# Optimization experiments

Hardware: AMD Instinct MI355X
Metric: run time of the kernel (lower is better)

Reference implementation:

```python
import jax, jax.numpy as jnp
import numpy as np

B, S, D = 4, 2048, 1024          # batch, seq, hidden_units
E, K, I = 16, 2, 1024            # n_routed_experts, top_k, moe_inter_dim
SH = 2                            # n_shared_experts -> shared inter = SH*I
ROUTE_SCALE = 1.0


def setup_inputs() -> dict:
    key = jax.random.key(0)
    ks = jax.random.split(key, 12)
    std = 0.02
    return {
        "x": jax.random.normal(ks[0], (B, S, D), jnp.float32),
        "gate_w": jax.random.normal(ks[1], (E, D), jnp.float32) * std,
        # expert weights, torch Linear layout [out, in], stacked over experts
        "w1": jax.random.normal(ks[2], (E, I, D), jnp.float32) * std,
        "w2": jax.random.normal(ks[3], (E, D, I), jnp.float32) * std,
        "w3": jax.random.normal(ks[4], (E, I, D), jnp.float32) * std,
        # shared expert MLP (bias=True, nn.Linear default)
        "sw1": jax.random.normal(ks[5], (SH * I, D), jnp.float32) * std,
        "sb1": jnp.zeros((SH * I,), jnp.float32),
        "sw2": jax.random.normal(ks[6], (D, SH * I), jnp.float32) * std,
        "sb2": jnp.zeros((D,), jnp.float32),
        "sw3": jax.random.normal(ks[7], (SH * I, D), jnp.float32) * std,
        "sb3": jnp.zeros((SH * I,), jnp.float32),
    }


def reference(x, gate_w, w1, w2, w3, sw1, sb1, sw2, sb2, sw3, sb3):
    orig_shape = x.shape
    xt = x.reshape(-1, D)                       # [T, D]
    T = xt.shape[0]

    # ---- Gate: sigmoid scores, top-k, normalized weights ----
    scores = jax.nn.sigmoid(xt @ gate_w.T)      # [T, E]
    topk_vals, topk_idx = jax.lax.top_k(scores, K)
    weights = topk_vals / topk_vals.sum(-1, keepdims=True) * ROUTE_SCALE  # [T, K]

    # dense per-token-per-expert combine weight (zero for unselected experts)
    onehot = jax.nn.one_hot(topk_idx, E, dtype=xt.dtype)  # [T, K, E]
    w_full = jnp.einsum('tk,tke->te', weights, onehot)    # [T, E]

    # ---- Routed experts: SwiGLU per expert, weighted combine ----
    y = jnp.zeros_like(xt)
    for e in range(E):  # fixed small structural loop over experts
        h = jax.nn.silu(xt @ w1[e].T) * (xt @ w3[e].T)    # [T, I]
        y = y + w_full[:, e:e + 1] * (h @ w2[e].T)

    # ---- Load-balancing auxiliary loss ----
    counts = jax.lax.stop_gradient(onehot.sum((0, 1)))    # tokens per expert (non-diff, as in torch)
    expert_probs = w_full.sum(0)                          # sum of routing weights per expert
    f_i = E * counts / (K * T)
    P_i = expert_probs / T
    L_ExpBal = (f_i * P_i).sum()

    # ---- Shared expert (dense SwiGLU MLP with bias) ----
    z = (jax.nn.silu(xt @ sw1.T + sb1) * (xt @ sw3.T + sb3)) @ sw2.T + sb2

    return (y + z).reshape(orig_shape), L_ExpBal
```

## Files before the change

kernel.cpp:

```cpp
#include <hip/hip_runtime.h>
#include <cstdint>
#include <cstddef>

typedef unsigned short ushort_t;
typedef __attribute__((ext_vector_type(8))) short bf16x8;
typedef __attribute__((ext_vector_type(8))) unsigned short u16x8;
typedef __attribute__((ext_vector_type(4))) float f32x4;

#define T_TOKENS 8192
#define DIM      1024
#define NEXP     16

static __device__ __forceinline__ unsigned short f2bf(float f) {
  union { float f; unsigned u; } v; v.f = f;
  unsigned r = v.u + 0x7FFFu + ((v.u >> 16) & 1u);
  return (unsigned short)(r >> 16);
}

static __device__ __forceinline__ void gload16(const void* g, void* l) {
  __builtin_amdgcn_global_load_lds(
      (const __attribute__((address_space(1))) unsigned int*)g,
      (__attribute__((address_space(3))) unsigned int*)l, 16, 0, 0);
}

static __device__ __forceinline__ void xcd_map(int bx, int by, int gy,
                                               int& rb, int& cb) {
  int lin = bx + (by << 6);
  int xcd = lin & 7;
  int c = lin >> 3;
  int gyd = gy >> 3;
  cb = xcd * gyd + (c >> 6);
  rb = c & 63;
}

__global__ __launch_bounds__(256) void k_cvt8(const float* __restrict__ in,
                                              ushort_t* __restrict__ outp) {
  size_t i = ((size_t)blockIdx.x * 256 + threadIdx.x) * 8;
  float4 a = *(const float4*)(in + i);
  float4 b = *(const float4*)(in + i + 4);
  u16x8 o;
  o[0]=f2bf(a.x); o[1]=f2bf(a.y); o[2]=f2bf(a.z); o[3]=f2bf(a.w);
  o[4]=f2bf(b.x); o[5]=f2bf(b.y); o[6]=f2bf(b.z); o[7]=f2bf(b.w);
  *(u16x8*)(outp + i) = o;
}

__global__ __launch_bounds__(256) void k_score(const float* __restrict__ x,
                                               const float* __restrict__ gw,
                                               int* __restrict__ sel0,
                                               int* __restrict__ sel1,
                                               float* __restrict__ w0o,
                                               float* __restrict__ w1o) {
  int lane = threadIdx.x & 63;
  int wv = threadIdx.x >> 6;
  int t = blockIdx.x * 4 + wv;
  float xv[16];
  const float* xr = x + (size_t)t * DIM + lane * 16;
#pragma unroll
  for (int j = 0; j < 16; j += 4) {
    float4 v = *(const float4*)(xr + j);
    xv[j] = v.x; xv[j+1] = v.y; xv[j+2] = v.z; xv[j+3] = v.w;
  }
  float sc[NEXP];
#pragma unroll
  for (int e = 0; e < NEXP; e++) {
    const float* gr = gw + (size_t)e * DIM + lane * 16;
    float a = 0.f;
#pragma unroll
    for (int j = 0; j < 16; j += 4) {
      float4 g = *(const float4*)(gr + j);
      a += xv[j]*g.x + xv[j+1]*g.y + xv[j+2]*g.z + xv[j+3]*g.w;
    }
#pragma unroll
    for (int o = 32; o > 0; o >>= 1) a += __shfl_xor(a, o, 64);
    sc[e] = 1.f / (1.f + expf(-a));
  }
  if (lane == 0) {
    float best = -1e30f, sec = -1e30f;
    int bi = 0, si = 0;
#pragma unroll
    for (int e = 0; e < NEXP; e++) {
      float s = sc[e];
      if (s > best) { sec = best; si = bi; best = s; bi = e; }
      else if (s > sec) { sec = s; si = e; }
    }
    float inv = 1.f / (best + sec);
    sel0[t] = bi; sel1[t] = si;
    w0o[t] = best * inv; w1o[t] = sec * inv;
  }
}

__global__ __launch_bounds__(256) void k_compact(const int* __restrict__ sel0,
                                                 const int* __restrict__ sel1,
                                                 const float* __restrict__ w0v,
                                                 const float* __restrict__ w1v,
                                                 int* __restrict__ toklist,
                                                 float* __restrict__ wlist,
                                                 int* __restrict__ cnt,
                                                 float* __restrict__ probs) {
  const int e = blockIdx.x;
  const int tid = threadIdx.x;
  const int lane = tid & 63, wv = tid >> 6;
  __shared__ int wbase[4];
  __shared__ int woff[4];
  __shared__ int base;
  __shared__ float pacc[4];
  if (tid == 0) base = 0;
  float myprob = 0.f;
  int* tl = toklist + e * T_TOKENS;
  float* wl = wlist + e * T_TOKENS;
  __syncthreads();
  for (int t0 = 0; t0 < T_TOKENS; t0 += 256) {
    int t = t0 + tid;
    bool m0 = (sel0[t] == e), m1 = (sel1[t] == e);
    bool m = m0 || m1;
    float wgt = m0 ? w0v[t] : (m1 ? w1v[t] : 0.f);
    unsigned long long bal = __ballot(m);
    int prefix = __popcll(bal & ((1ull << lane) - 1ull));
    if (lane == 0) wbase[wv] = __popcll(bal);
    __syncthreads();
    if (tid == 0) {
      int a = base;
#pragma unroll
      for (int i = 0; i < 4; i++) { woff[i] = a; a += wbase[i]; }
      base = a;
    }
    __syncthreads();
    if (m) {
      int pos = woff[wv] + prefix;
      tl[pos] = t;
      wl[pos] = wgt;
    }
    myprob += wgt;
  }
#pragma unroll
  for (int o = 32; o > 0; o >>= 1) myprob += __shfl_xor(myprob, o, 64);
  if (lane == 0) pacc[wv] = myprob;
  __syncthreads();
  if (tid == 0) {
    cnt[e] = base;
    probs[e] = pacc[0] + pacc[1] + pacc[2] + pacc[3];
  }
}

__global__ void k_offsets(const int* __restrict__ cnt, const float* __restrict__ probs,
                          int* __restrict__ seg, float* __restrict__ loss_out) {
  if (threadIdx.x == 0 && blockIdx.x == 0) {
    int acc = 0;
    float L = 0.f;
    for (int e = 0; e < NEXP; e++) {
      seg[e] = acc; acc += cnt[e];
      float f = 16.f * (float)cnt[e] / (2.f * 8192.f);
      L += f * (probs[e] / 8192.f);
    }
    seg[NEXP] = acc;
    *loss_out = L;
  }
}


__global__ __launch_bounds__(256, 3) void k_gemm1(
    const ushort_t* __restrict__ X,
    const ushort_t* __restrict__ W1b, const ushort_t* __restrict__ W3b,
    const float* __restrict__ b1, const float* __restrict__ b3,
    ushort_t* __restrict__ P, int ldP,
    const int* __restrict__ toklist, const int* __restrict__ cnt,
    const int* __restrict__ seg) {
  __shared__ __align__(16) ushort_t As[2 * 4096];
  __shared__ __align__(16) ushort_t B1s[2 * 2048];
  __shared__ __align__(16) ushort_t B3s[2 * 2048];

  const int tid = threadIdx.x;
  const int lane = tid & 63, wave = tid >> 6;
  const int wm = wave >> 1, wn = wave & 1;
  int rb, cb;
  xcd_map(blockIdx.x, blockIdx.y, gridDim.y, rb, cb);
  const int e = blockIdx.z;

  int Ne, pbase;
  const int* tl = nullptr;
  const ushort_t* W1 = W1b;
  const ushort_t* W3 = W3b;
  if (cnt) {
    Ne = cnt[e];
    if (rb * 128 >= Ne) return;
    pbase = seg[e];
    tl = toklist + e * T_TOKENS;
    W1 += (size_t)e * 1024 * 1024;
    W3 += (size_t)e * 1024 * 1024;
  } else { Ne = T_TOKENS; pbase = 0; }

  const int c0 = wave * 2, c1 = c0 + 1;
  const int lrow = lane >> 2;
  const int scol = (((lane & 3) ^ (lrow & 3))) * 8;

  const int ar0 = rb * 128 + c0 * 16 + lrow;
  const int ar1 = rb * 128 + c1 * 16 + lrow;
  const int sr0 = tl ? tl[min(ar0, Ne - 1)] : ar0;
  const int sr1 = tl ? tl[min(ar1, Ne - 1)] : ar1;
  const ushort_t* apA0 = X + (size_t)sr0 * DIM + scol;
  const ushort_t* apA1 = X + (size_t)sr1 * DIM + scol;

  const int brw = cb * 64 + wave * 16 + lrow;
  const ushort_t* bp1 = W1 + (size_t)brw * DIM + scol;
  const ushort_t* bp3 = W3 + (size_t)brw * DIM + scol;

  const int o0 = c0 * 512, o1 = c1 * 512;
  const int ow = wave * 512;

  f32x4 acc1[4][2], acc3[4][2];
#pragma unroll
  for (int m = 0; m < 4; m++)
#pragma unroll
    for (int n = 0; n < 2; n++) {
      acc1[m][n] = (f32x4){0.f, 0.f, 0.f, 0.f};
      acc3[m][n] = (f32x4){0.f, 0.f, 0.f, 0.f};
    }

  const int koff = (((lane >> 4) ^ (lane & 3))) * 8;

#define STAGE1(AB, BB, K0) { \
    gload16(apA0 + (K0), As  + (AB) + o0); \
    gload16(apA1 + (K0), As  + (AB) + o1); \
    gload16(bp1  + (K0), B1s + (BB) + ow); \
    gload16(bp3  + (K0), B3s + (BB) + ow); }

#define PHASE1(AC, BC, T, STG) { \
    if (STG) STAGE1(4096 - (AC), 2048 - (BC), ((T) + 1) * 32); \
    bf16x8 af[4], b1f[2], b3f[2]; \
    _Pragma("unroll") \
    for (int m = 0; m < 4; m++) { \
      int row = wm * 64 + m * 16 + (lane & 15); \
      af[m] = *(const bf16x8*)(As + (AC) + row * 32 + koff); } \
    _Pragma("unroll") \
    for (int n = 0; n < 2; n++) { \
      int rw = wn * 32 + n * 16 + (lane & 15); \
      b1f[n] = *(const bf16x8*)(B1s + (BC) + rw * 32 + koff); \
      b3f[n] = *(const bf16x8*)(B3s + (BC) + rw * 32 + koff); } \
    _Pragma("unroll") \
    for (int m = 0; m < 4; m++) \
      _Pragma("unroll") \
      for (int n = 0; n < 2; n++) { \
        acc1[m][n] = __builtin_amdgcn_mfma_f32_16x16x32_bf16(af[m], b1f[n], acc1[m][n], 0, 0, 0); \
        acc3[m][n] = __builtin_amdgcn_mfma_f32_16x16x32_bf16(af[m], b3f[n], acc3[m][n], 0, 0, 0); } \
    __syncthreads(); }

  STAGE1(0, 0, 0);
  __syncthreads();
  for (int kk = 0; kk < 30; kk += 2) {
    PHASE1(0, 0, kk, 1);
    PHASE1(4096, 2048, kk + 1, 1);
  }
  PHASE1(0, 0, 30, 1);
  PHASE1(4096, 2048, 31, 0);
#undef PHASE1
#undef STAGE1

#pragma unroll
  for (int n = 0; n < 2; n++) {
    int col = cb * 64 + wn * 32 + n * 16 + (lane & 15);
    float bb1 = b1 ? b1[col] : 0.f;
    float bb3 = b3 ? b3[col] : 0.f;
#pragma unroll
    for (int m = 0; m < 4; m++) {
#pragma unroll
      for (int r = 0; r < 4; r++) {
        int row = rb * 128 + wm * 64 + m * 16 + (lane >> 4) * 4 + r;
        if (row < Ne) {
          float h1 = acc1[m][n][r] + bb1;
          float h3 = acc3[m][n][r] + bb3;
          float pv = (h1 / (1.f + expf(-h1))) * h3;
          P[(size_t)(pbase + row) * ldP + col] = f2bf(pv);
        }
      }
    }
  }
}

__global__ __launch_bounds__(256, 3) void k_gemm2(
    const ushort_t* __restrict__ Pbuf, const ushort_t* __restrict__ W2b,
    const float* __restrict__ b2,
    float* __restrict__ outp,
    const int* __restrict__ toklist, const float* __restrict__ wlist,
    const int* __restrict__ cnt, const int* __restrict__ seg, int Kd) {
  __shared__ __align__(16) ushort_t As[2 * 4096];
  __shared__ __align__(16) ushort_t Bs[2 * 4096];

  const int tid = threadIdx.x;
  const int lane = tid & 63, wave = tid >> 6;
  const int wm = wave >> 1, wn = wave & 1;
  int rb, cb;
  xcd_map(blockIdx.x, blockIdx.y, gridDim.y, rb, cb);
  const int e = blockIdx.z;

  int Ne;
  const ushort_t* A;
  const ushort_t* W2 = W2b;
  const int* tl = nullptr; const float* wl = nullptr;
  if (cnt) {
    Ne = cnt[e];
    if (rb * 128 >= Ne) return;
    A = Pbuf + (size_t)seg[e] * Kd;
    W2 += (size_t)e * 1024 * Kd;
    tl = toklist + e * T_TOKENS;
    wl = wlist + e * T_TOKENS;
  } else { Ne = T_TOKENS; A = Pbuf; }

  const int c0 = wave * 2, c1 = c0 + 1;
  const int lrow = lane >> 2;
  const int scol = (((lane & 3) ^ (lrow & 3))) * 8;

  const int sr0 = min(rb * 128 + c0 * 16 + lrow, Ne - 1);
  const int sr1 = min(rb * 128 + c1 * 16 + lrow, Ne - 1);
  const ushort_t* apA0 = A + (size_t)sr0 * Kd + scol;
  const ushort_t* apA1 = A + (size_t)sr1 * Kd + scol;

  const int br0 = cb * 128 + c0 * 16 + lrow;
  const int br1 = cb * 128 + c1 * 16 + lrow;
  const ushort_t* bp0 = W2 + (size_t)br0 * Kd + scol;
  const ushort_t* bp1 = W2 + (size_t)br1 * Kd + scol;

  const int o0 = c0 * 512, o1 = c1 * 512;

  f32x4 acc[4][4];
#pragma unroll
  for (int m = 0; m < 4; m++)
#pragma unroll
    for (int n = 0; n < 4; n++) acc[m][n] = (f32x4){0.f, 0.f, 0.f, 0.f};

  const int koff = (((lane >> 4) ^ (lane & 3))) * 8;
  const int ksteps = Kd >> 5;

#define STAGE2(BUF, K0) { \
    gload16(apA0 + (K0), As + (BUF) + o0); \
    gload16(apA1 + (K0), As + (BUF) + o1); \
    gload16(bp0  + (K0), Bs + (BUF) + o0); \
    gload16(bp1  + (K0), Bs + (BUF) + o1); }

#define PHASE2(CUR, T, STG) { \
    if (STG) STAGE2(4096 - (CUR), ((T) + 1) * 32); \
    bf16x8 af[4], bf[4]; \
    _Pragma("unroll") \
    for (int m = 0; m < 4; m++) { \
      int row = wm * 64 + m * 16 + (lane & 15); \
      af[m] = *(const bf16x8*)(As + (CUR) + row * 32 + koff); } \
    _Pragma("unroll") \
    for (int n = 0; n < 4; n++) { \
      int rw = wn * 64 + n * 16 + (lane & 15); \
      bf[n] = *(const bf16x8*)(Bs + (CUR) + rw * 32 + koff); } \
    _Pragma("unroll") \
    for (int m = 0; m < 4; m++) \
      _Pragma("unroll") \
      for (int n = 0; n < 4; n++) \
        acc[m][n] = __builtin_amdgcn_mfma_f32_16x16x32_bf16(af[m], bf[n], acc[m][n], 0, 0, 0); \
    __syncthreads(); }

  STAGE2(0, 0);
  __syncthreads();
  for (int kk = 0; kk < ksteps - 2; kk += 2) {
    PHASE2(0, kk, 1);
    PHASE2(4096, kk + 1, 1);
  }
  PHASE2(0, ksteps - 2, 1);
  PHASE2(4096, ksteps - 1, 0);
#undef PHASE2
#undef STAGE2

#pragma unroll
  for (int n = 0; n < 4; n++) {
    int col = cb * 128 + wn * 64 + n * 16 + (lane & 15);
    float bias = b2 ? b2[col] : 0.f;
#pragma unroll
    for (int m = 0; m < 4; m++) {
#pragma unroll
      for (int r = 0; r < 4; r++) {
        int rl = rb * 128 + wm * 64 + m * 16 + (lane >> 4) * 4 + r;
        if (cnt) {
          if (rl < Ne) {
            int tok = tl[rl];
            float wgt = wl[rl];
            atomicAdd(outp + (size_t)tok * DIM + col, acc[m][n][r] * wgt);
          }
        } else {
          outp[(size_t)rl * DIM + col] = acc[m][n][r] + bias;
        }
      }
    }
  }
}

extern "C" void kernel_launch(void* const* d_in, const int* in_sizes, int n_in,
                              void* d_out, int out_size, void* d_ws, size_t ws_size,
                              hipStream_t stream) {
  const float* x   = (const float*)d_in[0];
  const float* gw  = (const float*)d_in[1];
  const float* w1  = (const float*)d_in[2];
  const float* w2  = (const float*)d_in[3];
  const float* w3  = (const float*)d_in[4];
  const float* sw1 = (const float*)d_in[5];
  const float* sb1 = (const float*)d_in[6];
  const float* sw2 = (const float*)d_in[7];
  const float* sb2 = (const float*)d_in[8];
  const float* sw3 = (const float*)d_in[9];
  const float* sb3 = (const float*)d_in[10];
  float* out  = (float*)d_out;
  float* loss = out + (size_t)T_TOKENS * DIM;

  const size_t NW = (size_t)NEXP * 1024 * 1024;
  const size_t NS = (size_t)2048 * 1024;

  char* w = (char*)d_ws;
  ushort_t* w1b  = (ushort_t*)w; w += NW * 2;
  ushort_t* w2b  = (ushort_t*)w; w += NW * 2;
  ushort_t* w3b  = (ushort_t*)w; w += NW * 2;
  ushort_t* sw1b = (ushort_t*)w; w += NS * 2;
  ushort_t* sw2b = (ushort_t*)w; w += NS * 2;
  ushort_t* sw3b = (ushort_t*)w; w += NS * 2;
  ushort_t* p_buf = (ushort_t*)w; w += (size_t)33554432 + 262144;
  ushort_t* x_bf  = (ushort_t*)w; w += (size_t)T_TOKENS * DIM * 2;
  int*   toklist  = (int*)w;      w += (size_t)NEXP * T_TOKENS * 4;
  float* wlist    = (float*)w;    w += (size_t)NEXP * T_TOKENS * 4;
  int*   sel0     = (int*)w;      w += (size_t)T_TOKENS * 4;
  int*   sel1     = (int*)w;      w += (size_t)T_TOKENS * 4;
  float* w0v      = (float*)w;    w += (size_t)T_TOKENS * 4;
  float* w1v      = (float*)w;    w += (size_t)T_TOKENS * 4;
  int*   cnt      = (int*)w;      w += 64;
  float* probs    = (float*)w;    w += 64;
  int*   seg      = (int*)w;      w += 128;

  k_cvt8<<<(T_TOKENS * DIM) / 2048, 256, 0, stream>>>(x, x_bf);
  k_cvt8<<<NW / 2048, 256, 0, stream>>>(w1, w1b);
  k_cvt8<<<NW / 2048, 256, 0, stream>>>(w2, w2b);
  k_cvt8<<<NW / 2048, 256, 0, stream>>>(w3, w3b);
  k_cvt8<<<NS / 2048, 256, 0, stream>>>(sw1, sw1b);
  k_cvt8<<<NS / 2048, 256, 0, stream>>>(sw2, sw2b);
  k_cvt8<<<NS / 2048, 256, 0, stream>>>(sw3, sw3b);

  k_score<<<T_TOKENS / 4, 256, 0, stream>>>(x, gw, sel0, sel1, w0v, w1v);
  k_compact<<<NEXP, 256, 0, stream>>>(sel0, sel1, w0v, w1v,
                                      toklist, wlist, cnt, probs);
  k_offsets<<<1, 64, 0, stream>>>(cnt, probs, seg, loss);

  k_gemm1<<<dim3(64, 32, 1), 256, 0, stream>>>(x_bf, sw1b, sw3b, sb1, sb3,
                                               p_buf, 2048, nullptr, nullptr, nullptr);
  k_gemm2<<<dim3(64, 8, 1), 256, 0, stream>>>(p_buf, sw2b, sb2, out,
                                              nullptr, nullptr, nullptr, nullptr, 2048);

  k_gemm1<<<dim3(64, 16, NEXP), 256, 0, stream>>>(x_bf, w1b, w3b, nullptr, nullptr,
                                                  p_buf, 1024, toklist, cnt, seg);
  k_gemm2<<<dim3(64, 8, NEXP), 256, 0, stream>>>(p_buf, w2b, nullptr, out,
                                                 toklist, wlist, cnt, seg, 1024);
}
```

Measured before the change: 596.2 us.

## Merge conversion launches and fuse shared-expert GEMMs into routed-expert grids

Replaces seven separate fp32-to-bf16 conversion launches with one kernel that picks the source tensor by block index. Folds the shared-expert GEMMs into the routed-expert launches as an extra z-slice, giving each a separate intermediate buffer when workspace allows. The output is zeroed up front and every slice accumulates with atomics. This removes launch overhead and tail idle time between the shared and routed phases, at the cost of an extra memset and atomic stores for the shared expert's output.

Measured after the change: 608.9 us. 2.1% more time.

```diff
diff --git a/kernel.cpp b/kernel.cpp
--- a/kernel.cpp
+++ b/kernel.cpp
@@ -33,15 +33,31 @@
   rb = c & 63;
 }
 
-__global__ __launch_bounds__(256) void k_cvt8(const float* __restrict__ in,
-                                              ushort_t* __restrict__ outp) {
-  size_t i = ((size_t)blockIdx.x * 256 + threadIdx.x) * 8;
-  float4 a = *(const float4*)(in + i);
-  float4 b = *(const float4*)(in + i + 4);
+__global__ __launch_bounds__(256) void k_cvt_all(
+    const float* __restrict__ x,  const float* __restrict__ w1,
+    const float* __restrict__ w2, const float* __restrict__ w3,
+    const float* __restrict__ sw1, const float* __restrict__ sw2,
+    const float* __restrict__ sw3,
+    ushort_t* __restrict__ xb,  ushort_t* __restrict__ w1b,
+    ushort_t* __restrict__ w2b, ushort_t* __restrict__ w3b,
+    ushort_t* __restrict__ sw1b, ushort_t* __restrict__ sw2b,
+    ushort_t* __restrict__ sw3b) {
+  int b = blockIdx.x;
+  const float* src; ushort_t* dst; int rel;
+  if (b < 4096)       { src = x;   dst = xb;   rel = b; }
+  else if (b < 12288) { src = w1;  dst = w1b;  rel = b - 4096; }
+  else if (b < 20480) { src = w2;  dst = w2b;  rel = b - 12288; }
+  else if (b < 28672) { src = w3;  dst = w3b;  rel = b - 20480; }
+  else if (b < 29696) { src = sw1; dst = sw1b; rel = b - 28672; }
+  else if (b < 30720) { src = sw2; dst = sw2b; rel = b - 29696; }
+  else                { src = sw3; dst = sw3b; rel = b - 30720; }
+  size_t i = ((size_t)rel * 256 + threadIdx.x) * 8;
+  float4 a = *(const float4*)(src + i);
+  float4 c = *(const float4*)(src + i + 4);
   u16x8 o;
   o[0]=f2bf(a.x); o[1]=f2bf(a.y); o[2]=f2bf(a.z); o[3]=f2bf(a.w);
-  o[4]=f2bf(b.x); o[5]=f2bf(b.y); o[6]=f2bf(b.z); o[7]=f2bf(b.w);
-  *(u16x8*)(outp + i) = o;
+  o[4]=f2bf(c.x); o[5]=f2bf(c.y); o[6]=f2bf(c.z); o[7]=f2bf(c.w);
+  *(u16x8*)(dst + i) = o;
 }
 
 __global__ __launch_bounds__(256) void k_score(const float* __restrict__ x,
@@ -157,14 +173,14 @@
   }
 }
 
-
 __global__ __launch_bounds__(256, 3) void k_gemm1(
     const ushort_t* __restrict__ X,
-    const ushort_t* __restrict__ W1b, const ushort_t* __restrict__ W3b,
-    const float* __restrict__ b1, const float* __restrict__ b3,
-    ushort_t* __restrict__ P, int ldP,
+    const ushort_t* __restrict__ w1b, const ushort_t* __restrict__ w3b,
+    const ushort_t* __restrict__ sw1b, const ushort_t* __restrict__ sw3b,
+    const float* __restrict__ sb1, const float* __restrict__ sb3,
+    ushort_t* __restrict__ Pr, ushort_t* __restrict__ Ps,
     const int* __restrict__ toklist, const int* __restrict__ cnt,
-    const int* __restrict__ seg) {
+    const int* __restrict__ seg, int zbase) {
   __shared__ __align__(16) ushort_t As[2 * 4096];
   __shared__ __align__(16) ushort_t B1s[2 * 2048];
   __shared__ __align__(16) ushort_t B3s[2 * 2048];
@@ -172,22 +188,29 @@
   const int tid = threadIdx.x;
   const int lane = tid & 63, wave = tid >> 6;
   const int wm = wave >> 1, wn = wave & 1;
-  int rb, cb;
-  xcd_map(blockIdx.x, blockIdx.y, gridDim.y, rb, cb);
-  const int e = blockIdx.z;
-
-  int Ne, pbase;
+  const int e = blockIdx.z + zbase;
+
+  int rb, cb, Ne, pbase, ldP;
   const int* tl = nullptr;
-  const ushort_t* W1 = W1b;
-  const ushort_t* W3 = W3b;
-  if (cnt) {
+  const ushort_t *W1, *W3;
+  const float *b1 = nullptr, *b3 = nullptr;
+  ushort_t* P;
+  if (e < NEXP) {
+    if (blockIdx.y >= 16) return;
+    xcd_map(blockIdx.x, blockIdx.y, 16, rb, cb);
     Ne = cnt[e];
     if (rb * 128 >= Ne) return;
     pbase = seg[e];
     tl = toklist + e * T_TOKENS;
-    W1 += (size_t)e * 1024 * 1024;
-    W3 += (size_t)e * 1024 * 1024;
-  } else { Ne = T_TOKENS; pbase = 0; }
+    W1 = w1b + (size_t)e * 1024 * 1024;
+    W3 = w3b + (size_t)e * 1024 * 1024;
+    P = Pr; ldP = 1024;
+  } else {
+    xcd_map(blockIdx.x, blockIdx.y, 32, rb, cb);
+    Ne = T_TOKENS; pbase = 0;
+    W1 = sw1b; W3 = sw3b; b1 = sb1; b3 = sb3;
+    P = Ps; ldP = 2048;
+  }
 
   const int c0 = wave * 2, c1 = c0 + 1;
   const int lrow = lane >> 2;
@@ -277,33 +300,38 @@
 }
 
 __global__ __launch_bounds__(256, 3) void k_gemm2(
-    const ushort_t* __restrict__ Pbuf, const ushort_t* __restrict__ W2b,
-    const float* __restrict__ b2,
+    const ushort_t* __restrict__ Pr, const ushort_t* __restrict__ Ps,
+    const ushort_t* __restrict__ w2b, const ushort_t* __restrict__ sw2b,
+    const float* __restrict__ sb2,
     float* __restrict__ outp,
     const int* __restrict__ toklist, const float* __restrict__ wlist,
-    const int* __restrict__ cnt, const int* __restrict__ seg, int Kd) {
+    const int* __restrict__ cnt, const int* __restrict__ seg, int zbase) {
   __shared__ __align__(16) ushort_t As[2 * 4096];
   __shared__ __align__(16) ushort_t Bs[2 * 4096];
 
   const int tid = threadIdx.x;
   const int lane = tid & 63, wave = tid >> 6;
   const int wm = wave >> 1, wn = wave & 1;
+  const int e = blockIdx.z + zbase;
   int rb, cb;
-  xcd_map(blockIdx.x, blockIdx.y, gridDim.y, rb, cb);
-  const int e = blockIdx.z;
-
-  int Ne;
-  const ushort_t* A;
-  const ushort_t* W2 = W2b;
+  xcd_map(blockIdx.x, blockIdx.y, 8, rb, cb);
+
+  int Ne, Kd;
+  const ushort_t *A, *W2;
   const int* tl = nullptr; const float* wl = nullptr;
-  if (cnt) {
+  const float* b2 = nullptr;
+  if (e < NEXP) {
     Ne = cnt[e];
     if (rb * 128 >= Ne) return;
-    A = Pbuf + (size_t)seg[e] * Kd;
-    W2 += (size_t)e * 1024 * Kd;
+    A = Pr + (size_t)seg[e] * 1024;
+    W2 = w2b + (size_t)e * 1024 * 1024;
     tl = toklist + e * T_TOKENS;
     wl = wlist + e * T_TOKENS;
-  } else { Ne = T_TOKENS; A = Pbuf; }
+    Kd = 1024;
+  } else {
+    Ne = T_TOKENS;
+    A = Ps; W2 = sw2b; b2 = sb2; Kd = 2048;
+  }
 
   const int c0 = wave * 2, c1 = c0 + 1;
   const int lrow = lane >> 2;
@@ -374,14 +402,14 @@
 #pragma unroll
       for (int r = 0; r < 4; r++) {
         int rl = rb * 128 + wm * 64 + m * 16 + (lane >> 4) * 4 + r;
-        if (cnt) {
+        if (e < NEXP) {
           if (rl < Ne) {
             int tok = tl[rl];
             float wgt = wl[rl];
             atomicAdd(outp + (size_t)tok * DIM + col, acc[m][n][r] * wgt);
           }
         } else {
-          outp[(size_t)rl * DIM + col] = acc[m][n][r] + bias;
+          atomicAdd(outp + (size_t)rl * DIM + col, acc[m][n][r] + bias);
         }
       }
     }
@@ -407,6 +435,7 @@
 
   const size_t NW = (size_t)NEXP * 1024 * 1024;
   const size_t NS = (size_t)2048 * 1024;
+  const size_t PSZ = (size_t)16384 * 1024 * 2;
 
   char* w = (char*)d_ws;
   ushort_t* w1b  = (ushort_t*)w; w += NW * 2;
@@ -415,38 +444,48 @@
   ushort_t* sw1b = (ushort_t*)w; w += NS * 2;
   ushort_t* sw2b = (ushort_t*)w; w += NS * 2;
   ushort_t* sw3b = (ushort_t*)w; w += NS * 2;
-  ushort_t* p_buf = (ushort_t*)w; w += (size_t)33554432 + 262144;
-  ushort_t* x_bf  = (ushort_t*)w; w += (size_t)T_TOKENS * DIM * 2;
-  int*   toklist  = (int*)w;      w += (size_t)NEXP * T_TOKENS * 4;
-  float* wlist    = (float*)w;    w += (size_t)NEXP * T_TOKENS * 4;
-  int*   sel0     = (int*)w;      w += (size_t)T_TOKENS * 4;
-  int*   sel1     = (int*)w;      w += (size_t)T_TOKENS * 4;
-  float* w0v      = (float*)w;    w += (size_t)T_TOKENS * 4;
-  float* w1v      = (float*)w;    w += (size_t)T_TOKENS * 4;
-  int*   cnt      = (int*)w;      w += 64;
-  float* probs    = (float*)w;    w += 64;
-  int*   seg      = (int*)w;      w += 128;
-
-  k_cvt8<<<(T_TOKENS * DIM) / 2048, 256, 0, stream>>>(x, x_bf);
-  k_cvt8<<<NW / 2048, 256, 0, stream>>>(w1, w1b);
-  k_cvt8<<<NW / 2048, 256, 0, stream>>>(w2, w2b);
-  k_cvt8<<<NW / 2048, 256, 0, stream>>>(w3, w3b);
-  k_cvt8<<<NS / 2048, 256, 0, stream>>>(sw1, sw1b);
-  k_cvt8<<<NS / 2048, 256, 0, stream>>>(sw2, sw2b);
-  k_cvt8<<<NS / 2048, 256, 0, stream>>>(sw3, sw3b);
+  ushort_t* Pr   = (ushort_t*)w; w += PSZ;
+  ushort_t* x_bf = (ushort_t*)w; w += (size_t)T_TOKENS * DIM * 2;
+  int*   toklist = (int*)w;      w += (size_t)NEXP * T_TOKENS * 4;
+  float* wlist   = (float*)w;    w += (size_t)NEXP * T_TOKENS * 4;
+  int*   sel0    = (int*)w;      w += (size_t)T_TOKENS * 4;
+  int*   sel1    = (int*)w;      w += (size_t)T_TOKENS * 4;
+  float* w0v     = (float*)w;    w += (size_t)T_TOKENS * 4;
+  float* w1v     = (float*)w;    w += (size_t)T_TOKENS * 4;
+  int*   cnt     = (int*)w;      w += 64;
+  float* probs   = (float*)w;    w += 64;
+  int*   seg     = (int*)w;      w += 128;
+
+  size_t used = (size_t)(w - (char*)d_ws);
+  bool fused = (used + PSZ + 1024) <= ws_size;
+  ushort_t* Ps = fused ? (ushort_t*)w : Pr;
+
+  hipMemsetAsync(d_out, 0, (size_t)out_size * 4, stream);
+
+  k_cvt_all<<<31744, 256, 0, stream>>>(x, w1, w2, w3, sw1, sw2, sw3,
+                                       x_bf, w1b, w2b, w3b, sw1b, sw2b, sw3b);
 
   k_score<<<T_TOKENS / 4, 256, 0, stream>>>(x, gw, sel0, sel1, w0v, w1v);
   k_compact<<<NEXP, 256, 0, stream>>>(sel0, sel1, w0v, w1v,
                                       toklist, wlist, cnt, probs);
   k_offsets<<<1, 64, 0, stream>>>(cnt, probs, seg, loss);
 
-  k_gemm1<<<dim3(64, 32, 1), 256, 0, stream>>>(x_bf, sw1b, sw3b, sb1, sb3,
-                                               p_buf, 2048, nullptr, nullptr, nullptr);
-  k_gemm2<<<dim3(64, 8, 1), 256, 0, stream>>>(p_buf, sw2b, sb2, out,
-                                              nullptr, nullptr, nullptr, nullptr, 2048);
-
-  k_gemm1<<<dim3(64, 16, NEXP), 256, 0, stream>>>(x_bf, w1b, w3b, nullptr, nullptr,
-                                                  p_buf, 1024, toklist, cnt, seg);
-  k_gemm2<<<dim3(64, 8, NEXP), 256, 0, stream>>>(p_buf, w2b, nullptr, out,
-                                                 toklist, wlist, cnt, seg, 1024);
-}
+  if (fused) {
+    k_gemm1<<<dim3(64, 32, 17), 256, 0, stream>>>(
+        x_bf, w1b, w3b, sw1b, sw3b, sb1, sb3, Pr, Ps,
+        toklist, cnt, seg, 0);
+    k_gemm2<<<dim3(64, 8, 17), 256, 0, stream>>>(
+        Pr, Ps, w2b, sw2b, sb2, out, toklist, wlist, cnt, seg, 0);
+  } else {
+    k_gemm1<<<dim3(64, 32, 1), 256, 0, stream>>>(
+        x_bf, w1b, w3b, sw1b, sw3b, sb1, sb3, Pr, Ps,
+        toklist, cnt, seg, 16);
+    k_gemm2<<<dim3(64, 8, 1), 256, 0, stream>>>(
+        Pr, Ps, w2b, sw2b, sb2, out, toklist, wlist, cnt, seg, 16);
+    k_gemm1<<<dim3(64, 16, 16), 256, 0, stream>>>(
+        x_bf, w1b, w3b, sw1b, sw3b, sb1, sb3, Pr, Ps,
+        toklist, cnt, seg, 0);
+    k_gemm2<<<dim3(64, 8, 16), 256, 0, stream>>>(
+        Pr, Ps, w2b, sw2b, sb2, out, toklist, wlist, cnt, seg, 0);
+  }
+}
```
